# Performance work log

Measured on AMD Instinct MI355X. Metric: run time of the kernel, lower is better.

Reference implementation:

```python
import jax, jax.numpy as jnp
import numpy as np

NUM_GROUPS = 8
GROUP_SIZE = 512
FEATURE_DIM = NUM_GROUPS * GROUP_SIZE
MIN_BITS, MAX_BITS, TARGET_BITS = 2.0, 4.0 * 2, 4.0  # min=2, max=8, target=4
BIT_LEVELS = jnp.array([2.0, 4.0, 8.0], dtype=jnp.float32)
LN_EPS = 1e-5


def setup_inputs() -> dict:
    key = jax.random.key(0)
    ks = jax.random.split(key, 10)
    B, T = 16, 2048
    H = NUM_GROUPS * 2  # hidden of bit predictor
    inv8 = 1.0 / np.sqrt(NUM_GROUPS)
    invH = 1.0 / np.sqrt(H)
    return {
        "importance_scores": jax.random.normal(ks[0], (B, T, FEATURE_DIM), jnp.float32),
        "u": jax.random.uniform(ks[1], (B, NUM_GROUPS), jnp.float32),
        "W1": jax.random.uniform(ks[2], (NUM_GROUPS, H), jnp.float32, -inv8, inv8),
        "b1": jax.random.uniform(ks[3], (H,), jnp.float32, -inv8, inv8),
        "ln_g": jnp.ones((H,), jnp.float32),
        "ln_b": jnp.zeros((H,), jnp.float32),
        "W2": jax.random.uniform(ks[4], (H, NUM_GROUPS), jnp.float32, -invH, invH),
        "b2": jax.random.uniform(ks[5], (NUM_GROUPS,), jnp.float32, -invH, invH),
        "bit_embeddings": jax.random.normal(ks[6], (3, GROUP_SIZE), jnp.float32),
    }


def reference(importance_scores, u, W1, b1, ln_g, ln_b, W2, b2, bit_embeddings):
    B = importance_scores.shape[0]
    # [B,T,D] -> [B,D] -> group means [B,G]
    imp = importance_scores.mean(axis=1)
    group_imp = imp.reshape(B, NUM_GROUPS, GROUP_SIZE).mean(axis=-1)

    # tiny MLP bit predictor: Linear -> GELU -> LayerNorm -> Linear
    h = group_imp @ W1 + b1
    h = jax.nn.gelu(h, approximate=False)
    mu = h.mean(axis=-1, keepdims=True)
    var = ((h - mu) ** 2).mean(axis=-1, keepdims=True)
    h = (h - mu) * jax.lax.rsqrt(var + LN_EPS) * ln_g + ln_b
    logits = h @ W2 + b2

    # training-mode Gumbel perturbation (temperature = 1.0)
    gumbel = -jnp.log(-jnp.log(u + 1e-8) + 1e-8)
    bit_probs = jax.nn.softmax(logits + gumbel, axis=-1)

    # constrained continuous allocation
    alloc = MIN_BITS + bit_probs * (MAX_BITS - MIN_BITS)
    budget = TARGET_BITS * NUM_GROUPS
    alloc = alloc * (budget / alloc.sum(axis=-1, keepdims=True))
    alloc = jnp.clip(alloc, MIN_BITS, MAX_BITS)

    # discretize to nearest bit level with straight-through gradient
    dist = jnp.abs(alloc[..., None] - BIT_LEVELS)  # [B,G,3]
    idx = jnp.argmin(dist, axis=-1)
    hard = BIT_LEVELS[idx]
    discrete_bits = hard + alloc - jax.lax.stop_gradient(alloc)  # value == hard

    # per-group soft codebook mix: softmax(exp(-|b - level|)) @ embeddings
    bit_w = jax.nn.softmax(jnp.exp(-jnp.abs(discrete_bits[..., None] - BIT_LEVELS)), axis=-1)
    embeddings = jnp.einsum("bgl,ld->bgd", bit_w, bit_embeddings)

    group_indices = jnp.broadcast_to(
        (jnp.arange(FEATURE_DIM) // GROUP_SIZE)[None, :], (B, FEATURE_DIM)
    )
    bitrate_loss = (discrete_bits.mean() - TARGET_BITS) ** 2
    diversity_bonus = -(bit_probs * jnp.log(bit_probs + 1e-8)).sum(axis=-1).mean()
    return (discrete_bits, group_indices, embeddings, bitrate_loss, diversity_bonus, bit_probs)
```

## Files before the change

kernel.cpp:

```cpp
#include <hip/hip_runtime.h>
#include <math.h>

#define B_DIM 16
#define T_DIM 2048
#define D_DIM 4096
#define G_DIM 8
#define GS    512
#define H_DIM 16
#define CHUNKS 16
#define NPARTIAL (B_DIM * G_DIM * CHUNKS)

#define OUT_DBITS   0
#define OUT_GIDX    128
#define OUT_EMB     65664
#define OUT_BLOSS   131200
#define OUT_DIV     131201
#define OUT_BPROBS  131202

__global__ __launch_bounds__(256) void k_reduce(const float* __restrict__ scores,
                                                double* __restrict__ partials) {
    const int bid   = blockIdx.x;
    const int pair  = bid >> 4;
    const int chunk = bid & 15;
    const int b = pair >> 3;
    const int g = pair & 7;
    const int tid = threadIdx.x;

    const float4* base = reinterpret_cast<const float4*>(
        scores + (size_t)b * T_DIM * D_DIM + (size_t)g * GS);
    const int t0 = chunk * 128;

    double acc = 0.0;
    #pragma unroll 4
    for (int it = 0; it < 64; ++it) {
        const int l = tid + it * 256;
        const int t = l >> 7;
        const int q = l & 127;
        float4 v = base[(size_t)(t0 + t) * (D_DIM / 4) + q];
        acc += (double)v.x + (double)v.y + (double)v.z + (double)v.w;
    }

    __shared__ double sd[256];
    sd[tid] = acc;
    __syncthreads();
    #pragma unroll
    for (int s = 128; s > 0; s >>= 1) {
        if (tid < s) sd[tid] += sd[tid + s];
        __syncthreads();
    }
    if (tid == 0) partials[bid] = sd[0];
}

__global__ __launch_bounds__(128) void k_mlp(const double* __restrict__ partials,
                                             const float* __restrict__ u,
                                             const float* __restrict__ W1,
                                             const float* __restrict__ b1,
                                             const float* __restrict__ ln_g,
                                             const float* __restrict__ ln_b,
                                             const float* __restrict__ W2,
                                             const float* __restrict__ b2,
                                             float* __restrict__ out,
                                             float* __restrict__ bitw) {
    __shared__ float gi[B_DIM * G_DIM];
    __shared__ float ent[B_DIM];
    __shared__ float bitsum[B_DIM];
    const int tid = threadIdx.x;

    if (tid < 128) {
        double s = 0.0;
        #pragma unroll
        for (int c = 0; c < CHUNKS; ++c) s += partials[tid * CHUNKS + c];
        gi[tid] = (float)(s * (1.0 / ((double)T_DIM * (double)GS)));
    }
    __syncthreads();

    if (tid < B_DIM) {
        const int b = tid;
        float h[H_DIM];
        #pragma unroll
        for (int i = 0; i < H_DIM; ++i) {
            float a = b1[i];
            #pragma unroll
            for (int g = 0; g < G_DIM; ++g) a += gi[b * G_DIM + g] * W1[g * H_DIM + i];
            h[i] = 0.5f * a * (1.0f + erff(a * 0.70710678118654752440f));
        }
        float mu = 0.f;
        #pragma unroll
        for (int i = 0; i < H_DIM; ++i) mu += h[i];
        mu *= (1.0f / (float)H_DIM);
        float var = 0.f;
        #pragma unroll
        for (int i = 0; i < H_DIM; ++i) { float d = h[i] - mu; var += d * d; }
        var *= (1.0f / (float)H_DIM);
        const float inv = rsqrtf(var + 1e-5f);
        #pragma unroll
        for (int i = 0; i < H_DIM; ++i) h[i] = (h[i] - mu) * inv * ln_g[i] + ln_b[i];

        float z[G_DIM];
        #pragma unroll
        for (int j = 0; j < G_DIM; ++j) {
            float a = b2[j];
            #pragma unroll
            for (int i = 0; i < H_DIM; ++i) a += h[i] * W2[i * G_DIM + j];
            const float uu = u[b * G_DIM + j];
            const float gum = -logf(-logf(uu + 1e-8f) + 1e-8f);
            z[j] = a + gum;
        }
        float m = z[0];
        #pragma unroll
        for (int j = 1; j < G_DIM; ++j) m = fmaxf(m, z[j]);
        float p[G_DIM]; float ssum = 0.f;
        #pragma unroll
        for (int j = 0; j < G_DIM; ++j) { p[j] = expf(z[j] - m); ssum += p[j]; }
        const float rs = 1.0f / ssum;

        float alloc[G_DIM]; float asum = 0.f;
        #pragma unroll
        for (int j = 0; j < G_DIM; ++j) {
            p[j] *= rs;
            alloc[j] = 2.0f + p[j] * 6.0f;
            asum += alloc[j];
        }
        const float scale = 32.0f / asum;

        float entb = 0.f, bs = 0.f;
        #pragma unroll
        for (int j = 0; j < G_DIM; ++j) {
            float a = alloc[j] * scale;
            a = fminf(fmaxf(a, 2.0f), 8.0f);
            const float hard = (a <= 3.0f) ? 2.0f : ((a <= 6.0f) ? 4.0f : 8.0f);
            out[OUT_DBITS + b * G_DIM + j]  = hard;
            out[OUT_BPROBS + b * G_DIM + j] = p[j];
            entb += p[j] * logf(p[j] + 1e-8f);
            bs += hard;
            const float x0 = expf(-fabsf(hard - 2.0f));
            const float x1 = expf(-fabsf(hard - 4.0f));
            const float x2 = expf(-fabsf(hard - 8.0f));
            const float mm = fmaxf(x0, fmaxf(x1, x2));
            const float e0 = expf(x0 - mm), e1 = expf(x1 - mm), e2 = expf(x2 - mm);
            const float ir = 1.0f / (e0 + e1 + e2);
            bitw[(b * G_DIM + j) * 3 + 0] = e0 * ir;
            bitw[(b * G_DIM + j) * 3 + 1] = e1 * ir;
            bitw[(b * G_DIM + j) * 3 + 2] = e2 * ir;
        }
        ent[b] = entb;
        bitsum[b] = bs;
    }
    __syncthreads();

    if (tid == 0) {
        float tb = 0.f, te = 0.f;
        #pragma unroll
        for (int b = 0; b < B_DIM; ++b) { tb += bitsum[b]; te += ent[b]; }
        const float mb = tb * (1.0f / (float)(B_DIM * G_DIM));
        out[OUT_BLOSS] = (mb - 4.0f) * (mb - 4.0f);
        out[OUT_DIV]   = -te * (1.0f / (float)B_DIM);
    }
}

__global__ __launch_bounds__(256) void k_emb(const float* __restrict__ bitw,
                                             const float* __restrict__ emb,
                                             float* __restrict__ out) {
    const int l = blockIdx.x * 256 + threadIdx.x;
    const int b   = l >> 10;
    const int rem = l & 1023;
    const int g   = rem >> 7;
    const int j4  = rem & 127;

    const float4* e4 = reinterpret_cast<const float4*>(emb);
    const float4 e0 = e4[0 * 128 + j4];
    const float4 e1 = e4[1 * 128 + j4];
    const float4 e2 = e4[2 * 128 + j4];
    const float w0 = bitw[(b * G_DIM + g) * 3 + 0];
    const float w1 = bitw[(b * G_DIM + g) * 3 + 1];
    const float w2 = bitw[(b * G_DIM + g) * 3 + 2];

    float4 r;
    r.x = w0 * e0.x + w1 * e1.x + w2 * e2.x;
    r.y = w0 * e0.y + w1 * e1.y + w2 * e2.y;
    r.z = w0 * e0.z + w1 * e1.z + w2 * e2.z;
    r.w = w0 * e0.w + w1 * e1.w + w2 * e2.w;

    float4* o4 = reinterpret_cast<float4*>(out);
    o4[(OUT_EMB / 4) + l] = r;

    const float gv = (float)g;
    o4[(OUT_GIDX / 4) + l] = make_float4(gv, gv, gv, gv);
}

extern "C" void kernel_launch(void* const* d_in, const int* in_sizes, int n_in,
                              void* d_out, int out_size, void* d_ws, size_t ws_size,
                              hipStream_t stream) {
    const float* scores = (const float*)d_in[0];
    const float* u      = (const float*)d_in[1];
    const float* W1     = (const float*)d_in[2];
    const float* b1     = (const float*)d_in[3];
    const float* ln_g   = (const float*)d_in[4];
    const float* ln_b   = (const float*)d_in[5];
    const float* W2     = (const float*)d_in[6];
    const float* b2     = (const float*)d_in[7];
    const float* emb    = (const float*)d_in[8];
    float* out = (float*)d_out;

    double* partials = (double*)d_ws;
    float*  bitw     = (float*)((char*)d_ws + NPARTIAL * sizeof(double));

    k_reduce<<<NPARTIAL, 256, 0, stream>>>(scores, partials);
    k_mlp<<<1, 128, 0, stream>>>(partials, u, W1, b1, ln_g, ln_b, W2, b2, out, bitw);
    k_emb<<<64, 256, 0, stream>>>(bitw, emb, out);
}
```

Before: 105.9 us.

## Reduce full contiguous rows per block and use wave shuffle reductions

Each reduce block now covers 16 full contiguous rows of 4096 floats for one batch, spanning all 8 groups, rather than a 2KB strip of one group over 128 rows. The aim is fully contiguous memory access. The shared-memory tree reduction is replaced with wavefront shuffle reductions, and each block writes 8 per-group partials. The grid stays at 2048 blocks, but the MLP kernel now sums 128 partials per (b,g) serially in a single thread each, which adds latency to that tail kernel.

```diff
diff --git a/kernel.cpp b/kernel.cpp
--- a/kernel.cpp
+++ b/kernel.cpp
@@ -7,7 +7,7 @@
 #define G_DIM 8
 #define GS    512
 #define H_DIM 16
-#define CHUNKS 16
+#define CHUNKS 128
 #define NPARTIAL (B_DIM * G_DIM * CHUNKS)
 
 #define OUT_DBITS   0
@@ -20,35 +20,45 @@
 __global__ __launch_bounds__(256) void k_reduce(const float* __restrict__ scores,
                                                 double* __restrict__ partials) {
     const int bid   = blockIdx.x;
-    const int pair  = bid >> 4;
-    const int chunk = bid & 15;
-    const int b = pair >> 3;
-    const int g = pair & 7;
-    const int tid = threadIdx.x;
+    const int b     = bid >> 7;
+    const int chunk = bid & 127;
+    const int tid   = threadIdx.x;
 
     const float4* base = reinterpret_cast<const float4*>(
-        scores + (size_t)b * T_DIM * D_DIM + (size_t)g * GS);
-    const int t0 = chunk * 128;
-
-    double acc = 0.0;
+        scores + (size_t)b * T_DIM * D_DIM + (size_t)chunk * 16 * D_DIM);
+
+    double a0 = 0.0, a1 = 0.0, a2 = 0.0, a3 = 0.0;
     #pragma unroll 4
-    for (int it = 0; it < 64; ++it) {
-        const int l = tid + it * 256;
-        const int t = l >> 7;
-        const int q = l & 127;
-        float4 v = base[(size_t)(t0 + t) * (D_DIM / 4) + q];
-        acc += (double)v.x + (double)v.y + (double)v.z + (double)v.w;
-    }
-
-    __shared__ double sd[256];
-    sd[tid] = acc;
+    for (int r = 0; r < 16; ++r) {
+        const float4* row = base + (size_t)r * (D_DIM / 4);
+        const float4 v0 = row[tid];
+        const float4 v1 = row[tid + 256];
+        const float4 v2 = row[tid + 512];
+        const float4 v3 = row[tid + 768];
+        a0 += (double)v0.x + (double)v0.y + (double)v0.z + (double)v0.w;
+        a1 += (double)v1.x + (double)v1.y + (double)v1.z + (double)v1.w;
+        a2 += (double)v2.x + (double)v2.y + (double)v2.z + (double)v2.w;
+        a3 += (double)v3.x + (double)v3.y + (double)v3.z + (double)v3.w;
+    }
+
+    const int lane = tid & 63;
+    const int wave = tid >> 6;
+    __shared__ double wsum[4][4];
+    double acc[4] = {a0, a1, a2, a3};
+    #pragma unroll
+    for (int p = 0; p < 4; ++p) {
+        double v = acc[p];
+        #pragma unroll
+        for (int off = 32; off > 0; off >>= 1) v += __shfl_down(v, off, 64);
+        if (lane == 0) wsum[wave][p] = v;
+    }
     __syncthreads();
-    #pragma unroll
-    for (int s = 128; s > 0; s >>= 1) {
-        if (tid < s) sd[tid] += sd[tid + s];
-        __syncthreads();
-    }
-    if (tid == 0) partials[bid] = sd[0];
+
+    if (tid < G_DIM) {
+        const int p  = tid >> 1;
+        const int w0 = (tid & 1) * 2;
+        partials[(size_t)(b * G_DIM + tid) * CHUNKS + chunk] = wsum[w0][p] + wsum[w0 + 1][p];
+    }
 }
 
 __global__ __launch_bounds__(128) void k_mlp(const double* __restrict__ partials,
@@ -69,7 +79,7 @@
     if (tid < 128) {
         double s = 0.0;
         #pragma unroll
-        for (int c = 0; c < CHUNKS; ++c) s += partials[tid * CHUNKS + c];
+        for (int c = 0; c < CHUNKS; ++c) s += partials[(size_t)tid * CHUNKS + c];
         gi[tid] = (float)(s * (1.0 / ((double)T_DIM * (double)GS)));
     }
     __syncthreads();
@@ -205,7 +215,7 @@
     double* partials = (double*)d_ws;
     float*  bitw     = (float*)((char*)d_ws + NPARTIAL * sizeof(double));
 
-    k_reduce<<<NPARTIAL, 256, 0, stream>>>(scores, partials);
+    k_reduce<<<B_DIM * CHUNKS, 256, 0, stream>>>(scores, partials);
     k_mlp<<<1, 128, 0, stream>>>(partials, u, W1, b1, ln_g, ln_b, W2, b2, out, bitw);
     k_emb<<<64, 256, 0, stream>>>(bitw, emb, out);
 }
```

Result: slower. 110.1 us (median of 4 runs) (+4.0%).
